# Kernel optimization log

Hardware: AMD Instinct MI355X
Metric: run time of the kernel (lower is better)

Reference implementation:

```python
import jax, jax.numpy as jnp
import numpy as np

N, T, HID, H = 2, 2048, 1024, 16
D = HID // H


def setup_inputs() -> dict:
    key = jax.random.key(0)
    ks = jax.random.split(key, 11)
    s = 1.0 / np.sqrt(HID)
    return {
        "q": jax.random.normal(ks[0], (N, T, HID), jnp.float32),
        "k": jax.random.normal(ks[1], (N, T, HID), jnp.float32),
        "v": jax.random.normal(ks[2], (N, T, HID), jnp.float32),
        "Wq": jax.random.normal(ks[3], (HID, HID), jnp.float32) * s,
        "bq": jnp.zeros((HID,), jnp.float32),
        "Wk": jax.random.normal(ks[4], (HID, HID), jnp.float32) * s,
        "bk": jnp.zeros((HID,), jnp.float32),
        "Wv": jax.random.normal(ks[5], (HID, HID), jnp.float32) * s,
        "bv": jnp.zeros((HID,), jnp.float32),
        "Wo": jax.random.normal(ks[6], (HID, HID), jnp.float32) * s,
        "bo": jnp.zeros((HID,), jnp.float32),
    }


def reference(q, k, v, Wq, bq, Wk, bk, Wv, bv, Wo, bo):
    n, t, _ = q.shape
    # Linear projections, then the original's quirky head split:
    # .view(N, H, T, D) directly from (N, T, H*D) (no transpose).
    qh = (q @ Wq + bq).reshape(n, H, t, D)
    kh = (k @ Wk + bk).reshape(n, H, t, D)
    vh = (v @ Wv + bv).reshape(n, H, t, D)
    # scores: (N, H, T, T), scaled by sqrt(hidden_size) (not head dim)
    scores = jnp.einsum("nhtd,nhsd->nhts", qh, kh) / jnp.sqrt(jnp.float32(HID))
    # faithful quirk: softmax over dim=1 (the head axis)
    attn = jax.nn.softmax(scores, axis=1)
    # dropout is identity (eval / drop_rate=0)
    out = jnp.einsum("nhts,nhsd->nhtd", attn, vh).reshape(n, t, H * D)
    return out @ Wo + bo
```

## Files before the change

kernel.cpp:

```cpp
#include <hip/hip_runtime.h>

typedef unsigned short u16;
typedef __bf16 bf16x8 __attribute__((ext_vector_type(8)));
typedef float f32x4 __attribute__((ext_vector_type(4)));

#define MFMA16 __builtin_amdgcn_mfma_f32_16x16x32_bf16

constexpr int NB = 2, TS = 2048, HD = 1024, NH = 16, DH = 64;
constexpr float SCALE = 0.03125f;

__device__ __forceinline__ u16 f2bf(float f) {
    union { float f; unsigned u; } v; v.f = f;
    unsigned r = v.u + 0x7FFFu + ((v.u >> 16) & 1u);
    return (u16)(r >> 16);
}
__device__ __forceinline__ float bf2f(u16 h) {
    union { unsigned u; float f; } v; v.u = ((unsigned)h) << 16;
    return v.f;
}
__device__ __forceinline__ bf16x8 ldb8(const u16* p) {
    return *reinterpret_cast<const bf16x8*>(p);
}
__device__ __forceinline__ void glds16(const u16* g, u16* l) {
    __builtin_amdgcn_global_load_lds(
        (const __attribute__((address_space(1))) unsigned int*)g,
        (__attribute__((address_space(3))) unsigned int*)l, 16, 0, 0);
}

#if defined(__has_builtin)
#  if __has_builtin(__builtin_amdgcn_cvt_pk_bf16_f32)
#    define HAVE_PKBF16 1
#  endif
#endif
#ifndef HAVE_PKBF16
#  define HAVE_PKBF16 0
#endif
__device__ __forceinline__ unsigned pk2(float a, float b) {
#if HAVE_PKBF16
    typedef __bf16 bf16x2 __attribute__((ext_vector_type(2)));
    bf16x2 r = __builtin_amdgcn_cvt_pk_bf16_f32(a, b);
    return __builtin_bit_cast(unsigned, r);
#else
    return (unsigned)f2bf(a) | ((unsigned)f2bf(b) << 16);
#endif
}

__global__ __launch_bounds__(256) void to_bf16(
    const float* __restrict__ a0, const float* __restrict__ a1, const float* __restrict__ a2,
    u16* __restrict__ o0, u16* __restrict__ o1, u16* __restrict__ o2)
{
    const float* s; u16* d;
    if (blockIdx.y == 0)      { s = a0; d = o0; }
    else if (blockIdx.y == 1) { s = a1; d = o1; }
    else                      { s = a2; d = o2; }
    size_t i = ((size_t)blockIdx.x * 256 + threadIdx.x) * 8;
    float4 v0 = *reinterpret_cast<const float4*>(s + i);
    float4 v1 = *reinterpret_cast<const float4*>(s + i + 4);
    uint4 w = { pk2(v0.x, v0.y), pk2(v0.z, v0.w), pk2(v1.x, v1.y), pk2(v1.z, v1.w) };
    *reinterpret_cast<uint4*>(d + i) = w;
}

__global__ __launch_bounds__(256) void wtrans(
    const float* __restrict__ w0, const float* __restrict__ w1,
    const float* __restrict__ w2, const float* __restrict__ w3,
    u16* __restrict__ o0, u16* __restrict__ o1,
    u16* __restrict__ o2, u16* __restrict__ o3)
{
    const float* src; u16* dst;
    if (blockIdx.z == 0)      { src = w0; dst = o0; }
    else if (blockIdx.z == 1) { src = w1; dst = o1; }
    else if (blockIdx.z == 2) { src = w2; dst = o2; }
    else                      { src = w3; dst = o3; }
    __shared__ __align__(16) u16 tile[64 * 72];
    const int k0 = blockIdx.y * 64, n0 = blockIdx.x * 64;
    const int t = threadIdx.x, r = t >> 2, c0 = (t & 3) << 4;
#pragma unroll
    for (int j = 0; j < 4; ++j) {
        float4 v = *reinterpret_cast<const float4*>(&src[(size_t)(k0 + r) * HD + n0 + c0 + 4 * j]);
        tile[(c0 + 4 * j + 0) * 72 + r] = f2bf(v.x);
        tile[(c0 + 4 * j + 1) * 72 + r] = f2bf(v.y);
        tile[(c0 + 4 * j + 2) * 72 + r] = f2bf(v.z);
        tile[(c0 + 4 * j + 3) * 72 + r] = f2bf(v.w);
    }
    __syncthreads();
#pragma unroll
    for (int j = 0; j < 2; ++j)
        *reinterpret_cast<uint4*>(&dst[(size_t)(n0 + r) * HD + k0 + c0 + 8 * j]) =
            *reinterpret_cast<const uint4*>(&tile[r * 72 + c0 + 8 * j]);
}

__global__ __launch_bounds__(256) void gemm_qkv(
    const u16* __restrict__ A0, const u16* __restrict__ A1, const u16* __restrict__ A2,
    const u16* __restrict__ B0, const u16* __restrict__ B1, const u16* __restrict__ B2,
    const float* __restrict__ c0, const float* __restrict__ c1, const float* __restrict__ c2,
    u16* __restrict__ C0, u16* __restrict__ C1, u16* __restrict__ C2)
{
    const u16 *A, *BT; const float* bias; u16* C;
    if (blockIdx.z == 0)      { A = A0; BT = B0; bias = c0; C = C0; }
    else if (blockIdx.z == 1) { A = A1; BT = B1; bias = c1; C = C1; }
    else                      { A = A2; BT = B2; bias = c2; C = C2; }
    constexpr int M = NB * TS, N = HD, K = HD;
    __shared__ __align__(16) u16 As[128 * 32];
    __shared__ __align__(16) u16 Bs[128 * 32];
    const int m0 = blockIdx.y * 128, n0 = blockIdx.x * 128;
    const int tid = threadIdx.x, wid = tid >> 6, lane = tid & 63;
    const int q = lane >> 4, c = lane & 15;
    const int wm = wid >> 1, wn = wid & 1;
    const int srow = tid >> 2, scol = (tid & 3) << 3;
    (void)M;
    f32x4 acc[4][4] = {};
    for (int k0 = 0; k0 < K; k0 += 32) {
        glds16(&A[(size_t)(m0 + srow) * K + k0 + scol],       &As[tid * 8]);
        glds16(&A[(size_t)(m0 + 64 + srow) * K + k0 + scol],  &As[2048 + tid * 8]);
        glds16(&BT[(size_t)(n0 + srow) * K + k0 + scol],      &Bs[tid * 8]);
        glds16(&BT[(size_t)(n0 + 64 + srow) * K + k0 + scol], &Bs[2048 + tid * 8]);
        __syncthreads();
        bf16x8 af[4], bf[4];
#pragma unroll
        for (int i = 0; i < 4; ++i)  af[i] = ldb8(&As[(wm * 64 + i * 16 + c) * 32 + q * 8]);
#pragma unroll
        for (int jn = 0; jn < 4; ++jn) bf[jn] = ldb8(&Bs[(wn * 64 + jn * 16 + c) * 32 + q * 8]);
#pragma unroll
        for (int i = 0; i < 4; ++i)
#pragma unroll
            for (int jn = 0; jn < 4; ++jn)
                acc[i][jn] = MFMA16(bf[jn], af[i], acc[i][jn], 0, 0, 0);
        __syncthreads();
    }
#pragma unroll
    for (int i = 0; i < 4; ++i)
#pragma unroll
        for (int jn = 0; jn < 4; ++jn) {
            int row = m0 + wm * 64 + i * 16 + c;
            int col = n0 + wn * 64 + jn * 16 + q * 4;
            float4 bb = *reinterpret_cast<const float4*>(&bias[col]);
            uint2 w = { pk2(acc[i][jn][0] + bb.x, acc[i][jn][1] + bb.y),
                        pk2(acc[i][jn][2] + bb.z, acc[i][jn][3] + bb.w) };
            *reinterpret_cast<uint2*>(&C[(size_t)row * N + col]) = w;
        }
}

__global__ __launch_bounds__(256) void gemm_out(
    const u16* __restrict__ A, const u16* __restrict__ BT,
    const float* __restrict__ bias, float* __restrict__ C,
    int M, int N, int K)
{
    __shared__ __align__(16) u16 As[64 * 32];
    __shared__ __align__(16) u16 Bs[128 * 32];
    const int m0 = blockIdx.y * 64, n0 = blockIdx.x * 128;
    const int tid = threadIdx.x, wid = tid >> 6, lane = tid & 63;
    const int q = lane >> 4, c = lane & 15;
    const int wm = wid >> 1, wn = wid & 1;
    const int arow = tid >> 2, acol = (tid & 3) << 3;
    f32x4 acc[2][4] = {};
    for (int k0 = 0; k0 < K; k0 += 32) {
        glds16(&A[(size_t)(m0 + arow) * K + k0 + acol], &As[tid * 8]);
        glds16(&BT[(size_t)(n0 + arow) * K + k0 + acol], &Bs[tid * 8]);
        glds16(&BT[(size_t)(n0 + 64 + arow) * K + k0 + acol], &Bs[2048 + tid * 8]);
        __syncthreads();
        bf16x8 af[2], bf[4];
#pragma unroll
        for (int jm = 0; jm < 2; ++jm) af[jm] = ldb8(&As[(wm * 32 + jm * 16 + c) * 32 + q * 8]);
#pragma unroll
        for (int jn = 0; jn < 4; ++jn) bf[jn] = ldb8(&Bs[(wn * 64 + jn * 16 + c) * 32 + q * 8]);
#pragma unroll
        for (int jm = 0; jm < 2; ++jm)
#pragma unroll
            for (int jn = 0; jn < 4; ++jn)
                acc[jm][jn] = MFMA16(bf[jn], af[jm], acc[jm][jn], 0, 0, 0);
        __syncthreads();
    }
#pragma unroll
    for (int jm = 0; jm < 2; ++jm)
#pragma unroll
        for (int jn = 0; jn < 4; ++jn) {
            int row = m0 + wm * 32 + jm * 16 + c;
            int col = n0 + wn * 64 + jn * 16 + q * 4;
            float4 bb = *reinterpret_cast<const float4*>(&bias[col]);
            float4 v = { acc[jm][jn][0] + bb.x, acc[jm][jn][1] + bb.y,
                         acc[jm][jn][2] + bb.z, acc[jm][jn][3] + bb.w };
            *reinterpret_cast<float4*>(&C[(size_t)row * N + col]) = v;
        }
}

__global__ __launch_bounds__(256) void vtrans(const u16* __restrict__ V, u16* __restrict__ VT)
{
    __shared__ __align__(16) u16 tile[64 * 72];
    const int nh = blockIdx.y, t0 = blockIdx.x * 64;
    const u16* src = V + (size_t)nh * TS * DH;
    u16* dst = VT + (size_t)nh * DH * TS;
    const int t = threadIdx.x, r = t >> 2, c0 = (t & 3) << 4;
    *reinterpret_cast<uint4*>(&tile[r * 72 + c0]) =
        *reinterpret_cast<const uint4*>(&src[(size_t)(t0 + r) * DH + c0]);
    *reinterpret_cast<uint4*>(&tile[r * 72 + c0 + 8]) =
        *reinterpret_cast<const uint4*>(&src[(size_t)(t0 + r) * DH + c0 + 8]);
    __syncthreads();
    const int d = t >> 2, tc = (t & 3) << 4;
    u16 tmp[16];
#pragma unroll
    for (int j = 0; j < 16; ++j) tmp[j] = tile[(tc + j) * 72 + d];
    *reinterpret_cast<uint4*>(&dst[(size_t)d * TS + t0 + tc]) = *reinterpret_cast<const uint4*>(&tmp[0]);
    *reinterpret_cast<uint4*>(&dst[(size_t)d * TS + t0 + tc + 8]) = *reinterpret_cast<const uint4*>(&tmp[8]);
}

__global__ __launch_bounds__(256) void z_kernel(
    const u16* __restrict__ Qp, const u16* __restrict__ Kp, u16* __restrict__ Zf)
{
    __shared__ __align__(16) u16 Ks[64 * 64];
    const int sb = blockIdx.x, tb = blockIdx.y, n = blockIdx.z;
    const int s0 = sb * 64, t0 = tb * 128;
    const int tid = threadIdx.x, wid = tid >> 6, lane = tid & 63;
    const int q = lane >> 4, c = lane & 15;
    const int krow = tid >> 3, kch = tid & 7;
    float zacc[2][4][4] = {};
    for (int h = 0; h < NH; ++h) {
        const u16* Qh = Qp + (size_t)(n * NH + h) * TS * DH;
        const u16* Kh = Kp + (size_t)(n * NH + h) * TS * DH;
        glds16(&Kh[(size_t)(s0 + krow) * DH + ((kch ^ (krow & 7)) << 3)], &Ks[tid * 8]);
        glds16(&Kh[(size_t)(s0 + 32 + krow) * DH + ((kch ^ (krow & 7)) << 3)], &Ks[2048 + tid * 8]);
        __syncthreads();
        bf16x8 qa[2][2], kb[4][2];
#pragma unroll
        for (int jm = 0; jm < 2; ++jm)
#pragma unroll
            for (int kf = 0; kf < 2; ++kf)
                qa[jm][kf] = ldb8(&Qh[(size_t)(t0 + wid * 32 + jm * 16 + c) * DH + kf * 32 + q * 8]);
#pragma unroll
        for (int i = 0; i < 4; ++i)
#pragma unroll
            for (int kf = 0; kf < 2; ++kf)
                kb[i][kf] = ldb8(&Ks[(i * 16 + c) * 64 + (((kf * 4 + q) ^ (c & 7)) << 3)]);
        f32x4 s_[2][4] = {};
#pragma unroll
        for (int kf = 0; kf < 2; ++kf)
#pragma unroll
            for (int jm = 0; jm < 2; ++jm)
#pragma unroll
                for (int i = 0; i < 4; ++i)
                    s_[jm][i] = MFMA16(kb[i][kf], qa[jm][kf], s_[jm][i], 0, 0, 0);
#pragma unroll
        for (int jm = 0; jm < 2; ++jm)
#pragma unroll
            for (int i = 0; i < 4; ++i)
#pragma unroll
                for (int r = 0; r < 4; ++r)
                    zacc[jm][i][r] += __expf(s_[jm][i][r] * SCALE);
        __syncthreads();
    }
    size_t chunk = ((size_t)((n * 32 + sb) * 16 + tb)) * 8192 + wid * 2048 + lane * 32;
#pragma unroll
    for (int jm = 0; jm < 2; ++jm) {
        unsigned w32[8];
#pragma unroll
        for (int i = 0; i < 4; ++i) {
            w32[i * 2 + 0] = pk2(1.0f / zacc[jm][i][0], 1.0f / zacc[jm][i][1]);
            w32[i * 2 + 1] = pk2(1.0f / zacc[jm][i][2], 1.0f / zacc[jm][i][3]);
        }
        *reinterpret_cast<uint4*>(&Zf[chunk + jm * 16])     = *reinterpret_cast<const uint4*>(&w32[0]);
        *reinterpret_cast<uint4*>(&Zf[chunk + jm * 16 + 8]) = *reinterpret_cast<const uint4*>(&w32[4]);
    }
}

__global__ __launch_bounds__(256) void attn_kernel(
    const u16* __restrict__ Qp, const u16* __restrict__ Kp, const u16* __restrict__ VT,
    const u16* __restrict__ Zf, u16* __restrict__ o2)
{
    __shared__ __align__(16) u16 Ks[64 * 64];
    __shared__ __align__(16) u16 Vs[64 * 64];
    __shared__ __align__(16) u16 Ps[128 * 72];
    const int tb = blockIdx.x, h = blockIdx.y, n = blockIdx.z;
    const int t0 = tb * 128;
    const int tid = threadIdx.x, wid = tid >> 6, lane = tid & 63;
    const int q = lane >> 4, c = lane & 15;
    const int krow = tid >> 3, kch = tid & 7;
    const size_t base = (size_t)(n * NH + h) * TS * DH;
    const u16* Qh = Qp + base; const u16* Kh = Kp + base; const u16* VTh = VT + base;
    bf16x8 qa[2][2];
#pragma unroll
    for (int jm = 0; jm < 2; ++jm)
#pragma unroll
        for (int kf = 0; kf < 2; ++kf)
            qa[jm][kf] = ldb8(&Qh[(size_t)(t0 + wid * 32 + jm * 16 + c) * DH + kf * 32 + q * 8]);
    f32x4 oacc[2][4] = {};
    for (int sb = 0; sb < 32; ++sb) {
        const int s0 = sb * 64;
        glds16(&Kh[(size_t)(s0 + krow) * DH + ((kch ^ (krow & 7)) << 3)], &Ks[tid * 8]);
        glds16(&Kh[(size_t)(s0 + 32 + krow) * DH + ((kch ^ (krow & 7)) << 3)], &Ks[2048 + tid * 8]);
        glds16(&VTh[(size_t)krow * TS + s0 + ((kch ^ (krow & 7)) << 3)], &Vs[tid * 8]);
        glds16(&VTh[(size_t)(32 + krow) * TS + s0 + ((kch ^ (krow & 7)) << 3)], &Vs[2048 + tid * 8]);
        __syncthreads();
        bf16x8 kb[4][2];
#pragma unroll
        for (int i = 0; i < 4; ++i)
#pragma unroll
            for (int kf = 0; kf < 2; ++kf)
                kb[i][kf] = ldb8(&Ks[(i * 16 + c) * 64 + (((kf * 4 + q) ^ (c & 7)) << 3)]);
        f32x4 s_[2][4] = {};
#pragma unroll
        for (int kf = 0; kf < 2; ++kf)
#pragma unroll
            for (int jm = 0; jm < 2; ++jm)
#pragma unroll
                for (int i = 0; i < 4; ++i)
                    s_[jm][i] = MFMA16(kb[i][kf], qa[jm][kf], s_[jm][i], 0, 0, 0);
        size_t chunk = ((size_t)((n * 32 + sb) * 16 + tb)) * 8192 + wid * 2048 + lane * 32;
        u16 zl[32];
        *reinterpret_cast<uint4*>(&zl[0])  = *reinterpret_cast<const uint4*>(&Zf[chunk]);
        *reinterpret_cast<uint4*>(&zl[8])  = *reinterpret_cast<const uint4*>(&Zf[chunk + 8]);
        *reinterpret_cast<uint4*>(&zl[16]) = *reinterpret_cast<const uint4*>(&Zf[chunk + 16]);
        *reinterpret_cast<uint4*>(&zl[24]) = *reinterpret_cast<const uint4*>(&Zf[chunk + 24]);
#pragma unroll
        for (int jm = 0; jm < 2; ++jm)
#pragma unroll
            for (int i = 0; i < 4; ++i) {
                float p0 = __expf(s_[jm][i][0] * SCALE) * bf2f(zl[jm * 16 + i * 4 + 0]);
                float p1 = __expf(s_[jm][i][1] * SCALE) * bf2f(zl[jm * 16 + i * 4 + 1]);
                float p2 = __expf(s_[jm][i][2] * SCALE) * bf2f(zl[jm * 16 + i * 4 + 2]);
                float p3 = __expf(s_[jm][i][3] * SCALE) * bf2f(zl[jm * 16 + i * 4 + 3]);
                uint2 w = { pk2(p0, p1), pk2(p2, p3) };
                *reinterpret_cast<uint2*>(&Ps[(wid * 32 + jm * 16 + c) * 72 + i * 16 + q * 4]) = w;
            }
        bf16x8 pa[2][2], vb[4][2];
#pragma unroll
        for (int jm = 0; jm < 2; ++jm)
#pragma unroll
            for (int kf = 0; kf < 2; ++kf)
                pa[jm][kf] = ldb8(&Ps[(wid * 32 + jm * 16 + c) * 72 + kf * 32 + q * 8]);
#pragma unroll
        for (int dn = 0; dn < 4; ++dn)
#pragma unroll
            for (int kf = 0; kf < 2; ++kf)
                vb[dn][kf] = ldb8(&Vs[(dn * 16 + c) * 64 + (((kf * 4 + q) ^ (c & 7)) << 3)]);
#pragma unroll
        for (int kf = 0; kf < 2; ++kf)
#pragma unroll
            for (int jm = 0; jm < 2; ++jm)
#pragma unroll
                for (int dn = 0; dn < 4; ++dn)
                    oacc[jm][dn] = MFMA16(vb[dn][kf], pa[jm][kf], oacc[jm][dn], 0, 0, 0);
        __syncthreads();
    }
#pragma unroll
    for (int jm = 0; jm < 2; ++jm)
#pragma unroll
        for (int dn = 0; dn < 4; ++dn) {
            int t = t0 + wid * 32 + jm * 16 + c;
            int d = dn * 16 + q * 4;
            uint2 w = { pk2(oacc[jm][dn][0], oacc[jm][dn][1]),
                        pk2(oacc[jm][dn][2], oacc[jm][dn][3]) };
            *reinterpret_cast<uint2*>(&o2[base + (size_t)t * DH + d]) = w;
        }
}

extern "C" void kernel_launch(void* const* d_in, const int* in_sizes, int n_in,
                              void* d_out, int out_size, void* d_ws, size_t ws_size,
                              hipStream_t stream)
{
    const float* q  = (const float*)d_in[0];
    const float* k  = (const float*)d_in[1];
    const float* v  = (const float*)d_in[2];
    const float* Wq = (const float*)d_in[3];
    const float* bq = (const float*)d_in[4];
    const float* Wk = (const float*)d_in[5];
    const float* bk = (const float*)d_in[6];
    const float* Wv = (const float*)d_in[7];
    const float* bv = (const float*)d_in[8];
    const float* Wo = (const float*)d_in[9];
    const float* bo = (const float*)d_in[10];
    float* out = (float*)d_out;

    u16* ws  = (u16*)d_ws;
    u16* wqT = ws + 0 * 1048576;
    u16* wkT = ws + 1 * 1048576;
    u16* wvT = ws + 2 * 1048576;
    u16* woT = ws + 3 * 1048576;
    u16* S1  = ws + 4194304;
    u16* S2  = S1 + 4194304;
    u16* S3  = S2 + 4194304;
    u16* S4  = S3 + 4194304;
    u16* S5  = S4 + 4194304;
    u16* S6  = S5 + 4194304;
    (void)S3;
    u16 *qb = S1, *kb = S2, *vb = S3;
    u16 *Qp = S4, *Kp = S5, *Vp = S6;
    u16 *VTb = S1, *Zf = S2, *o2 = S6;

    to_bf16<<<dim3(2048, 3), 256, 0, stream>>>(q, k, v, qb, kb, vb);
    wtrans<<<dim3(16, 16, 4), 256, 0, stream>>>(Wq, Wk, Wv, Wo, wqT, wkT, wvT, woT);
    gemm_qkv<<<dim3(8, 32, 3), 256, 0, stream>>>(qb, kb, vb, wqT, wkT, wvT,
                                                 bq, bk, bv, Qp, Kp, Vp);
    vtrans<<<dim3(32, 32), 256, 0, stream>>>(Vp, VTb);
    z_kernel<<<dim3(32, 16, 2), 256, 0, stream>>>(Qp, Kp, Zf);
    attn_kernel<<<dim3(16, 16, 2), 256, 0, stream>>>(Qp, Kp, VTb, Zf, o2);
    gemm_out<<<dim3(8, 64), 256, 0, stream>>>(o2, woT, bo, out, NB * TS, HD, HD);
}
```

Measured before the change: 324.0 us.

## Fold softmax scale into Wq, fuse V transpose into QKV GEMM, retile attention

Pre-multiplies Wq (and bq in the epilogue) by scale*log2(e), so both z_kernel and attn_kernel can use a raw exp2 with no per-element multiply. The V projection epilogue now writes directly in the transposed head layout, which removes the separate vtrans kernel but replaces vectorized stores with scattered 2-byte writes. z_kernel stages Q tiles through swizzled LDS instead of reading them straight from global memory. The Z buffer layout is changed to per-row contiguous, and attention blocks are halved to 64 query rows, giving twice as many blocks with less per-thread state.

New measurement: 304.1 us. 1.07x faster.

```diff
diff --git a/kernel.cpp b/kernel.cpp
--- a/kernel.cpp
+++ b/kernel.cpp
@@ -7,7 +7,7 @@
 #define MFMA16 __builtin_amdgcn_mfma_f32_16x16x32_bf16
 
 constexpr int NB = 2, TS = 2048, HD = 1024, NH = 16, DH = 64;
-constexpr float SCALE = 0.03125f;
+constexpr float ALPHA = 0.045084220027780106f;
 
 __device__ __forceinline__ u16 f2bf(float f) {
     union { float f; unsigned u; } v; v.f = f;
@@ -31,9 +31,15 @@
 #  if __has_builtin(__builtin_amdgcn_cvt_pk_bf16_f32)
 #    define HAVE_PKBF16 1
 #  endif
+#  if __has_builtin(__builtin_amdgcn_exp2f)
+#    define HAVE_EXP2 1
+#  endif
 #endif
 #ifndef HAVE_PKBF16
 #  define HAVE_PKBF16 0
+#endif
+#ifndef HAVE_EXP2
+#  define HAVE_EXP2 0
 #endif
 __device__ __forceinline__ unsigned pk2(float a, float b) {
 #if HAVE_PKBF16
@@ -42,6 +48,13 @@
     return __builtin_bit_cast(unsigned, r);
 #else
     return (unsigned)f2bf(a) | ((unsigned)f2bf(b) << 16);
+#endif
+}
+__device__ __forceinline__ float fexp2(float x) {
+#if HAVE_EXP2
+    return __builtin_amdgcn_exp2f(x);
+#else
+    return exp2f(x);
 #endif
 }
 
@@ -66,21 +79,21 @@
     u16* __restrict__ o0, u16* __restrict__ o1,
     u16* __restrict__ o2, u16* __restrict__ o3)
 {
-    const float* src; u16* dst;
-    if (blockIdx.z == 0)      { src = w0; dst = o0; }
-    else if (blockIdx.z == 1) { src = w1; dst = o1; }
-    else if (blockIdx.z == 2) { src = w2; dst = o2; }
-    else                      { src = w3; dst = o3; }
+    const float* src; u16* dst; float sc;
+    if (blockIdx.z == 0)      { src = w0; dst = o0; sc = ALPHA; }
+    else if (blockIdx.z == 1) { src = w1; dst = o1; sc = 1.0f; }
+    else if (blockIdx.z == 2) { src = w2; dst = o2; sc = 1.0f; }
+    else                      { src = w3; dst = o3; sc = 1.0f; }
     __shared__ __align__(16) u16 tile[64 * 72];
     const int k0 = blockIdx.y * 64, n0 = blockIdx.x * 64;
     const int t = threadIdx.x, r = t >> 2, c0 = (t & 3) << 4;
 #pragma unroll
     for (int j = 0; j < 4; ++j) {
         float4 v = *reinterpret_cast<const float4*>(&src[(size_t)(k0 + r) * HD + n0 + c0 + 4 * j]);
-        tile[(c0 + 4 * j + 0) * 72 + r] = f2bf(v.x);
-        tile[(c0 + 4 * j + 1) * 72 + r] = f2bf(v.y);
-        tile[(c0 + 4 * j + 2) * 72 + r] = f2bf(v.z);
-        tile[(c0 + 4 * j + 3) * 72 + r] = f2bf(v.w);
+        tile[(c0 + 4 * j + 0) * 72 + r] = f2bf(v.x * sc);
+        tile[(c0 + 4 * j + 1) * 72 + r] = f2bf(v.y * sc);
+        tile[(c0 + 4 * j + 2) * 72 + r] = f2bf(v.z * sc);
+        tile[(c0 + 4 * j + 3) * 72 + r] = f2bf(v.w * sc);
     }
     __syncthreads();
 #pragma unroll
@@ -93,13 +106,13 @@
     const u16* __restrict__ A0, const u16* __restrict__ A1, const u16* __restrict__ A2,
     const u16* __restrict__ B0, const u16* __restrict__ B1, const u16* __restrict__ B2,
     const float* __restrict__ c0, const float* __restrict__ c1, const float* __restrict__ c2,
-    u16* __restrict__ C0, u16* __restrict__ C1, u16* __restrict__ C2)
-{
-    const u16 *A, *BT; const float* bias; u16* C;
-    if (blockIdx.z == 0)      { A = A0; BT = B0; bias = c0; C = C0; }
-    else if (blockIdx.z == 1) { A = A1; BT = B1; bias = c1; C = C1; }
-    else                      { A = A2; BT = B2; bias = c2; C = C2; }
-    constexpr int M = NB * TS, N = HD, K = HD;
+    u16* __restrict__ C0, u16* __restrict__ C1, u16* __restrict__ VT)
+{
+    const u16 *A, *BT; const float* bias;
+    if (blockIdx.z == 0)      { A = A0; BT = B0; bias = c0; }
+    else if (blockIdx.z == 1) { A = A1; BT = B1; bias = c1; }
+    else                      { A = A2; BT = B2; bias = c2; }
+    constexpr int N = HD, K = HD;
     __shared__ __align__(16) u16 As[128 * 32];
     __shared__ __align__(16) u16 Bs[128 * 32];
     const int m0 = blockIdx.y * 128, n0 = blockIdx.x * 128;
@@ -107,7 +120,6 @@
     const int q = lane >> 4, c = lane & 15;
     const int wm = wid >> 1, wn = wid & 1;
     const int srow = tid >> 2, scol = (tid & 3) << 3;
-    (void)M;
     f32x4 acc[4][4] = {};
     for (int k0 = 0; k0 < K; k0 += 32) {
         glds16(&A[(size_t)(m0 + srow) * K + k0 + scol],       &As[tid * 8]);
@@ -127,17 +139,37 @@
                 acc[i][jn] = MFMA16(bf[jn], af[i], acc[i][jn], 0, 0, 0);
         __syncthreads();
     }
-#pragma unroll
-    for (int i = 0; i < 4; ++i)
-#pragma unroll
-        for (int jn = 0; jn < 4; ++jn) {
-            int row = m0 + wm * 64 + i * 16 + c;
-            int col = n0 + wn * 64 + jn * 16 + q * 4;
-            float4 bb = *reinterpret_cast<const float4*>(&bias[col]);
-            uint2 w = { pk2(acc[i][jn][0] + bb.x, acc[i][jn][1] + bb.y),
-                        pk2(acc[i][jn][2] + bb.z, acc[i][jn][3] + bb.w) };
-            *reinterpret_cast<uint2*>(&C[(size_t)row * N + col]) = w;
-        }
+    if (blockIdx.z == 2) {
+#pragma unroll
+        for (int i = 0; i < 4; ++i)
+#pragma unroll
+            for (int jn = 0; jn < 4; ++jn) {
+                int row = m0 + wm * 64 + i * 16 + c;
+                int nn = row >> 11, tp = row & 2047;
+                int col = n0 + wn * 64 + jn * 16 + q * 4;
+                int hh  = tp >> 7;
+                int tau = ((tp & 127) << 4) + (col >> 6);
+                int d0  = col & 63;
+#pragma unroll
+                for (int r = 0; r < 4; ++r)
+                    VT[(size_t)((nn * 16 + hh) * 64 + d0 + r) * 2048 + tau] =
+                        f2bf(acc[i][jn][r] + bias[col + r]);
+            }
+    } else {
+        u16* C = (blockIdx.z == 0) ? C0 : C1;
+        const float bsc = (blockIdx.z == 0) ? ALPHA : 1.0f;
+#pragma unroll
+        for (int i = 0; i < 4; ++i)
+#pragma unroll
+            for (int jn = 0; jn < 4; ++jn) {
+                int row = m0 + wm * 64 + i * 16 + c;
+                int col = n0 + wn * 64 + jn * 16 + q * 4;
+                float4 bb = *reinterpret_cast<const float4*>(&bias[col]);
+                uint2 w = { pk2(acc[i][jn][0] + bb.x * bsc, acc[i][jn][1] + bb.y * bsc),
+                            pk2(acc[i][jn][2] + bb.z * bsc, acc[i][jn][3] + bb.w * bsc) };
+                *reinterpret_cast<uint2*>(&C[(size_t)row * N + col]) = w;
+            }
+    }
 }
 
 __global__ __launch_bounds__(256) void gemm_out(
@@ -183,30 +215,11 @@
         }
 }
 
-__global__ __launch_bounds__(256) void vtrans(const u16* __restrict__ V, u16* __restrict__ VT)
-{
-    __shared__ __align__(16) u16 tile[64 * 72];
-    const int nh = blockIdx.y, t0 = blockIdx.x * 64;
-    const u16* src = V + (size_t)nh * TS * DH;
-    u16* dst = VT + (size_t)nh * DH * TS;
-    const int t = threadIdx.x, r = t >> 2, c0 = (t & 3) << 4;
-    *reinterpret_cast<uint4*>(&tile[r * 72 + c0]) =
-        *reinterpret_cast<const uint4*>(&src[(size_t)(t0 + r) * DH + c0]);
-    *reinterpret_cast<uint4*>(&tile[r * 72 + c0 + 8]) =
-        *reinterpret_cast<const uint4*>(&src[(size_t)(t0 + r) * DH + c0 + 8]);
-    __syncthreads();
-    const int d = t >> 2, tc = (t & 3) << 4;
-    u16 tmp[16];
-#pragma unroll
-    for (int j = 0; j < 16; ++j) tmp[j] = tile[(tc + j) * 72 + d];
-    *reinterpret_cast<uint4*>(&dst[(size_t)d * TS + t0 + tc]) = *reinterpret_cast<const uint4*>(&tmp[0]);
-    *reinterpret_cast<uint4*>(&dst[(size_t)d * TS + t0 + tc + 8]) = *reinterpret_cast<const uint4*>(&tmp[8]);
-}
-
 __global__ __launch_bounds__(256) void z_kernel(
     const u16* __restrict__ Qp, const u16* __restrict__ Kp, u16* __restrict__ Zf)
 {
     __shared__ __align__(16) u16 Ks[64 * 64];
+    __shared__ __align__(16) u16 Qs[128 * 64];
     const int sb = blockIdx.x, tb = blockIdx.y, n = blockIdx.z;
     const int s0 = sb * 64, t0 = tb * 128;
     const int tid = threadIdx.x, wid = tid >> 6, lane = tid & 63;
@@ -218,13 +231,17 @@
         const u16* Kh = Kp + (size_t)(n * NH + h) * TS * DH;
         glds16(&Kh[(size_t)(s0 + krow) * DH + ((kch ^ (krow & 7)) << 3)], &Ks[tid * 8]);
         glds16(&Kh[(size_t)(s0 + 32 + krow) * DH + ((kch ^ (krow & 7)) << 3)], &Ks[2048 + tid * 8]);
+#pragma unroll
+        for (int L = 0; L < 4; ++L)
+            glds16(&Qh[(size_t)(t0 + L * 32 + krow) * DH + ((kch ^ (krow & 7)) << 3)],
+                   &Qs[L * 2048 + tid * 8]);
         __syncthreads();
         bf16x8 qa[2][2], kb[4][2];
 #pragma unroll
         for (int jm = 0; jm < 2; ++jm)
 #pragma unroll
             for (int kf = 0; kf < 2; ++kf)
-                qa[jm][kf] = ldb8(&Qh[(size_t)(t0 + wid * 32 + jm * 16 + c) * DH + kf * 32 + q * 8]);
+                qa[jm][kf] = ldb8(&Qs[(wid * 32 + jm * 16 + c) * 64 + (((kf * 4 + q) ^ (c & 7)) << 3)]);
 #pragma unroll
         for (int i = 0; i < 4; ++i)
 #pragma unroll
@@ -244,20 +261,21 @@
             for (int i = 0; i < 4; ++i)
 #pragma unroll
                 for (int r = 0; r < 4; ++r)
-                    zacc[jm][i][r] += __expf(s_[jm][i][r] * SCALE);
-        __syncthreads();
-    }
-    size_t chunk = ((size_t)((n * 32 + sb) * 16 + tb)) * 8192 + wid * 2048 + lane * 32;
+                    zacc[jm][i][r] += fexp2(s_[jm][i][r]);
+        __syncthreads();
+    }
 #pragma unroll
     for (int jm = 0; jm < 2; ++jm) {
+        int t = t0 + wid * 32 + jm * 16 + c;
+        size_t zb = ((size_t)((n * 32 + sb) * 2048) + t) * 64 + q * 16;
         unsigned w32[8];
 #pragma unroll
         for (int i = 0; i < 4; ++i) {
             w32[i * 2 + 0] = pk2(1.0f / zacc[jm][i][0], 1.0f / zacc[jm][i][1]);
             w32[i * 2 + 1] = pk2(1.0f / zacc[jm][i][2], 1.0f / zacc[jm][i][3]);
         }
-        *reinterpret_cast<uint4*>(&Zf[chunk + jm * 16])     = *reinterpret_cast<const uint4*>(&w32[0]);
-        *reinterpret_cast<uint4*>(&Zf[chunk + jm * 16 + 8]) = *reinterpret_cast<const uint4*>(&w32[4]);
+        *reinterpret_cast<uint4*>(&Zf[zb])     = *reinterpret_cast<const uint4*>(&w32[0]);
+        *reinterpret_cast<uint4*>(&Zf[zb + 8]) = *reinterpret_cast<const uint4*>(&w32[4]);
     }
 }
 
@@ -267,27 +285,30 @@
 {
     __shared__ __align__(16) u16 Ks[64 * 64];
     __shared__ __align__(16) u16 Vs[64 * 64];
-    __shared__ __align__(16) u16 Ps[128 * 72];
+    __shared__ __align__(16) u16 Ps[64 * 72];
     const int tb = blockIdx.x, h = blockIdx.y, n = blockIdx.z;
-    const int t0 = tb * 128;
+    const int t0 = tb * 64;
     const int tid = threadIdx.x, wid = tid >> 6, lane = tid & 63;
     const int q = lane >> 4, c = lane & 15;
     const int krow = tid >> 3, kch = tid & 7;
     const size_t base = (size_t)(n * NH + h) * TS * DH;
     const u16* Qh = Qp + base; const u16* Kh = Kp + base; const u16* VTh = VT + base;
-    bf16x8 qa[2][2];
-#pragma unroll
-    for (int jm = 0; jm < 2; ++jm)
-#pragma unroll
-        for (int kf = 0; kf < 2; ++kf)
-            qa[jm][kf] = ldb8(&Qh[(size_t)(t0 + wid * 32 + jm * 16 + c) * DH + kf * 32 + q * 8]);
-    f32x4 oacc[2][4] = {};
+    const int tme = t0 + wid * 16 + c;
+    bf16x8 qa[2];
+#pragma unroll
+    for (int kf = 0; kf < 2; ++kf)
+        qa[kf] = ldb8(&Qh[(size_t)tme * DH + kf * 32 + q * 8]);
+    f32x4 oacc[4] = {};
     for (int sb = 0; sb < 32; ++sb) {
         const int s0 = sb * 64;
         glds16(&Kh[(size_t)(s0 + krow) * DH + ((kch ^ (krow & 7)) << 3)], &Ks[tid * 8]);
         glds16(&Kh[(size_t)(s0 + 32 + krow) * DH + ((kch ^ (krow & 7)) << 3)], &Ks[2048 + tid * 8]);
         glds16(&VTh[(size_t)krow * TS + s0 + ((kch ^ (krow & 7)) << 3)], &Vs[tid * 8]);
         glds16(&VTh[(size_t)(32 + krow) * TS + s0 + ((kch ^ (krow & 7)) << 3)], &Vs[2048 + tid * 8]);
+        size_t zb = ((size_t)((n * 32 + sb) * 2048) + tme) * 64 + q * 16;
+        u16 zl[16];
+        *reinterpret_cast<uint4*>(&zl[0]) = *reinterpret_cast<const uint4*>(&Zf[zb]);
+        *reinterpret_cast<uint4*>(&zl[8]) = *reinterpret_cast<const uint4*>(&Zf[zb + 8]);
         __syncthreads();
         bf16x8 kb[4][2];
 #pragma unroll
@@ -295,37 +316,25 @@
 #pragma unroll
             for (int kf = 0; kf < 2; ++kf)
                 kb[i][kf] = ldb8(&Ks[(i * 16 + c) * 64 + (((kf * 4 + q) ^ (c & 7)) << 3)]);
-        f32x4 s_[2][4] = {};
+        f32x4 s_[4] = {};
 #pragma unroll
         for (int kf = 0; kf < 2; ++kf)
 #pragma unroll
-            for (int jm = 0; jm < 2; ++jm)
-#pragma unroll
-                for (int i = 0; i < 4; ++i)
-                    s_[jm][i] = MFMA16(kb[i][kf], qa[jm][kf], s_[jm][i], 0, 0, 0);
-        size_t chunk = ((size_t)((n * 32 + sb) * 16 + tb)) * 8192 + wid * 2048 + lane * 32;
-        u16 zl[32];
-        *reinterpret_cast<uint4*>(&zl[0])  = *reinterpret_cast<const uint4*>(&Zf[chunk]);
-        *reinterpret_cast<uint4*>(&zl[8])  = *reinterpret_cast<const uint4*>(&Zf[chunk + 8]);
-        *reinterpret_cast<uint4*>(&zl[16]) = *reinterpret_cast<const uint4*>(&Zf[chunk + 16]);
-        *reinterpret_cast<uint4*>(&zl[24]) = *reinterpret_cast<const uint4*>(&Zf[chunk + 24]);
-#pragma unroll
-        for (int jm = 0; jm < 2; ++jm)
-#pragma unroll
-            for (int i = 0; i < 4; ++i) {
-                float p0 = __expf(s_[jm][i][0] * SCALE) * bf2f(zl[jm * 16 + i * 4 + 0]);
-                float p1 = __expf(s_[jm][i][1] * SCALE) * bf2f(zl[jm * 16 + i * 4 + 1]);
-                float p2 = __expf(s_[jm][i][2] * SCALE) * bf2f(zl[jm * 16 + i * 4 + 2]);
-                float p3 = __expf(s_[jm][i][3] * SCALE) * bf2f(zl[jm * 16 + i * 4 + 3]);
-                uint2 w = { pk2(p0, p1), pk2(p2, p3) };
-                *reinterpret_cast<uint2*>(&Ps[(wid * 32 + jm * 16 + c) * 72 + i * 16 + q * 4]) = w;
-            }
-        bf16x8 pa[2][2], vb[4][2];
-#pragma unroll
-        for (int jm = 0; jm < 2; ++jm)
-#pragma unroll
-            for (int kf = 0; kf < 2; ++kf)
-                pa[jm][kf] = ldb8(&Ps[(wid * 32 + jm * 16 + c) * 72 + kf * 32 + q * 8]);
+            for (int i = 0; i < 4; ++i)
+                s_[i] = MFMA16(kb[i][kf], qa[kf], s_[i], 0, 0, 0);
+#pragma unroll
+        for (int i = 0; i < 4; ++i) {
+            float p0 = fexp2(s_[i][0]) * bf2f(zl[i * 4 + 0]);
+            float p1 = fexp2(s_[i][1]) * bf2f(zl[i * 4 + 1]);
+            float p2 = fexp2(s_[i][2]) * bf2f(zl[i * 4 + 2]);
+            float p3 = fexp2(s_[i][3]) * bf2f(zl[i * 4 + 3]);
+            uint2 w = { pk2(p0, p1), pk2(p2, p3) };
+            *reinterpret_cast<uint2*>(&Ps[(wid * 16 + c) * 72 + i * 16 + q * 4]) = w;
+        }
+        bf16x8 pa[2], vb[4][2];
+#pragma unroll
+        for (int kf = 0; kf < 2; ++kf)
+            pa[kf] = ldb8(&Ps[(wid * 16 + c) * 72 + kf * 32 + q * 8]);
 #pragma unroll
         for (int dn = 0; dn < 4; ++dn)
 #pragma unroll
@@ -334,22 +343,15 @@
 #pragma unroll
         for (int kf = 0; kf < 2; ++kf)
 #pragma unroll
-            for (int jm = 0; jm < 2; ++jm)
-#pragma unroll
-                for (int dn = 0; dn < 4; ++dn)
-                    oacc[jm][dn] = MFMA16(vb[dn][kf], pa[jm][kf], oacc[jm][dn], 0, 0, 0);
-        __syncthreads();
-    }
-#pragma unroll
-    for (int jm = 0; jm < 2; ++jm)
-#pragma unroll
-        for (int dn = 0; dn < 4; ++dn) {
-            int t = t0 + wid * 32 + jm * 16 + c;
-            int d = dn * 16 + q * 4;
-            uint2 w = { pk2(oacc[jm][dn][0], oacc[jm][dn][1]),
-                        pk2(oacc[jm][dn][2], oacc[jm][dn][3]) };
-            *reinterpret_cast<uint2*>(&o2[base + (size_t)t * DH + d]) = w;
-        }
+            for (int dn = 0; dn < 4; ++dn)
+                oacc[dn] = MFMA16(vb[dn][kf], pa[kf], oacc[dn], 0, 0, 0);
+        __syncthreads();
+    }
+#pragma unroll
+    for (int dn = 0; dn < 4; ++dn) {
+        uint2 w = { pk2(oacc[dn][0], oacc[dn][1]), pk2(oacc[dn][2], oacc[dn][3]) };
+        *reinterpret_cast<uint2*>(&o2[base + (size_t)tme * DH + dn * 16 + q * 4]) = w;
+    }
 }
 
 extern "C" void kernel_launch(void* const* d_in, const int* in_sizes, int n_in,
@@ -380,17 +382,15 @@
     u16* S4  = S3 + 4194304;
     u16* S5  = S4 + 4194304;
     u16* S6  = S5 + 4194304;
-    (void)S3;
     u16 *qb = S1, *kb = S2, *vb = S3;
-    u16 *Qp = S4, *Kp = S5, *Vp = S6;
-    u16 *VTb = S1, *Zf = S2, *o2 = S6;
+    u16 *Qp = S4, *Kp = S5, *VTb = S6;
+    u16 *Zf = S1, *o2 = S3;
 
     to_bf16<<<dim3(2048, 3), 256, 0, stream>>>(q, k, v, qb, kb, vb);
     wtrans<<<dim3(16, 16, 4), 256, 0, stream>>>(Wq, Wk, Wv, Wo, wqT, wkT, wvT, woT);
     gemm_qkv<<<dim3(8, 32, 3), 256, 0, stream>>>(qb, kb, vb, wqT, wkT, wvT,
-                                                 bq, bk, bv, Qp, Kp, Vp);
-    vtrans<<<dim3(32, 32), 256, 0, stream>>>(Vp, VTb);
+                                                 bq, bk, bv, Qp, Kp, VTb);
     z_kernel<<<dim3(32, 16, 2), 256, 0, stream>>>(Qp, Kp, Zf);
-    attn_kernel<<<dim3(16, 16, 2), 256, 0, stream>>>(Qp, Kp, VTb, Zf, o2);
+    attn_kernel<<<dim3(32, 16, 2), 256, 0, stream>>>(Qp, Kp, VTb, Zf, o2);
     gemm_out<<<dim3(8, 64), 256, 0, stream>>>(o2, woT, bo, out, NB * TS, HD, HD);
 }
```
